# Kernel tuning notes

Hardware: AMD Instinct MI355X
Metric: run time of the kernel (lower is better)

The kernel has to match this reference:

```python
import jax, jax.numpy as jnp
import numpy as np

K = 1024
D = 64
BETA = 0.25


def setup_inputs() -> dict:
    key = jax.random.key(0)
    k1, k2 = jax.random.split(key)
    x = jax.random.normal(k1, (32, D, 64, 64), dtype=jnp.float32)
    # torch init: uniform(-1/K, 1/K)
    emb = jax.random.uniform(k2, (K, D), dtype=jnp.float32, minval=-1.0 / K, maxval=1.0 / K)
    return {"x": x, "emb": emb}


def reference(x, emb):
    B, C, H, W = x.shape
    z = jnp.transpose(x, (0, 2, 3, 1))          # [B,H,W,D]
    zf = z.reshape(-1, C)                        # [N,D]
    # squared euclidean distances ||z||^2 + ||e||^2 - 2 z.e
    dist = (jnp.sum(zf * zf, axis=1, keepdims=True)
            + jnp.sum(emb * emb, axis=1)
            - 2.0 * jnp.matmul(zf, emb.T))       # [N,K]
    min_idx = jnp.argmin(dist, axis=1)           # [N]
    # one-hot @ emb == gather
    z_q = emb[min_idx].reshape(z.shape)          # [B,H,W,D]
    sg = jax.lax.stop_gradient
    embedding_loss = (jnp.mean((sg(z_q) - z) ** 2)
                      + BETA * jnp.mean((z_q - sg(z)) ** 2))
    z_q_st = z + sg(z_q - z)                     # straight-through
    # code-usage perplexity
    n = zf.shape[0]
    e_mean = jnp.bincount(min_idx, length=K).astype(z.dtype) / n
    perplexity = jnp.exp(-jnp.sum(e_mean * jnp.log(e_mean + 1e-10)))
    z_q_out = jnp.transpose(z_q_st, (0, 3, 1, 2))  # [B,D,H,W]
    return embedding_loss, z_q_out, perplexity
```

## Files before the change

kernel.cpp:

```cpp
#include <hip/hip_runtime.h>
#include <math.h>

#define D_    64
#define K_    1024
#define N_    131072
#define HW_   4096
#define TAU   4e-5f

typedef unsigned long long ull;
typedef unsigned short ushort;
typedef short  bf16x8  __attribute__((ext_vector_type(8)));
typedef float  f32x4   __attribute__((ext_vector_type(4)));
typedef ushort ushort8 __attribute__((ext_vector_type(8)));

__device__ __forceinline__ ushort f2bf(float f) {
    unsigned u = __float_as_uint(f);
    return (ushort)((u + 0x7FFFu + ((u >> 16) & 1u)) >> 16);
}
__device__ __forceinline__ float b2f(ushort h) {
    return __uint_as_float((unsigned)h << 16);
}

__global__ __launch_bounds__(256)
void vq_prep(const float* __restrict__ emb, ushort* __restrict__ ehg,
             ushort* __restrict__ elg, float* __restrict__ e2g,
             float* __restrict__ embT, int* __restrict__ hist,
             int* __restrict__ cnt, double* __restrict__ ssqd) {
    const int n = blockIdx.x * 256 + threadIdx.x;
    if (n < K_) {
        const float* er = emb + (size_t)n * D_;
        float e2 = 0.0f;
        #pragma unroll
        for (int d8 = 0; d8 < 8; ++d8) {
            ushort8 hh, ll;
            #pragma unroll
            for (int j = 0; j < 8; ++j) {
                float e = er[d8 * 8 + j];
                e2 = fmaf(e, e, e2);
                ushort h = f2bf(e);
                hh[j] = h;
                ll[j] = f2bf(e - b2f(h));
                embT[(size_t)(d8 * 8 + j) * K_ + n] = e;
            }
            *(ushort8*)(ehg + (size_t)n * D_ + d8 * 8) = hh;
            *(ushort8*)(elg + (size_t)n * D_ + d8 * 8) = ll;
        }
        e2g[n] = e2;
        hist[n] = 0;
    }
    if (n == 0 && blockIdx.x == 0) { *cnt = 0; *ssqd = 0.0; }
}

#define LOADB(KT, BH0, BH1, BL0, BL1, E2)                                     \
    {                                                                         \
        int c_ = (kbase + (KT)) * 16 + c16;                                   \
        const ushort* eb_ = ehg + (size_t)c_ * D_ + g * 8;                    \
        BH0 = *(const bf16x8*)(eb_);                                          \
        BH1 = *(const bf16x8*)(eb_ + 32);                                     \
        const ushort* lb_ = elg + (size_t)c_ * D_ + g * 8;                    \
        BL0 = *(const bf16x8*)(lb_);                                          \
        BL1 = *(const bf16x8*)(lb_ + 32);                                     \
        E2 = e2g[c_];                                                         \
    }

#define COMPUTE(KT, BH0, BH1, BL0, BL1, E2)                                   \
    {                                                                         \
        const int c_ = (kbase + (KT)) * 16 + c16;                             \
        f32x4 ac[4];                                                          \
        _Pragma("unroll")                                                     \
        for (int t = 0; t < 4; ++t) {                                         \
            f32x4 a = {0.0f, 0.0f, 0.0f, 0.0f};                               \
            a = __builtin_amdgcn_mfma_f32_16x16x32_bf16(ah[t][0], BH0, a, 0, 0, 0); \
            a = __builtin_amdgcn_mfma_f32_16x16x32_bf16(al[t][0], BH0, a, 0, 0, 0); \
            a = __builtin_amdgcn_mfma_f32_16x16x32_bf16(ah[t][1], BH1, a, 0, 0, 0); \
            a = __builtin_amdgcn_mfma_f32_16x16x32_bf16(al[t][1], BH1, a, 0, 0, 0); \
            a = __builtin_amdgcn_mfma_f32_16x16x32_bf16(ah[t][0], BL0, a, 0, 0, 0); \
            a = __builtin_amdgcn_mfma_f32_16x16x32_bf16(ah[t][1], BL1, a, 0, 0, 0); \
            ac[t] = a;                                                        \
        }                                                                     \
        _Pragma("unroll")                                                     \
        for (int t = 0; t < 4; ++t) {                                         \
            _Pragma("unroll")                                                 \
            for (int q = 0; q < 4; ++q) {                                     \
                float dist = fmaf(-2.0f, ac[t][q], E2);                       \
                const int st = t * 4 + q;                                     \
                float vmax = fmaxf(dist, v1[st]);                             \
                bool lt = dist < v1[st];                                      \
                k1[st] = lt ? c_ : k1[st];                                    \
                v1[st] = fminf(dist, v1[st]);                                 \
                v2[st] = fminf(v2[st], vmax);                                 \
            }                                                                 \
        }                                                                     \
    }

__global__ __launch_bounds__(256)
void vq_mfma(const float* __restrict__ x, const float* __restrict__ emb,
             const ushort* __restrict__ ehg, const ushort* __restrict__ elg,
             const float* __restrict__ e2g, float* __restrict__ zq_out,
             int* __restrict__ list, int* __restrict__ cnt,
             int* __restrict__ hist, double* __restrict__ ssqd) {
    __shared__ float lv1[4][64], lv2[4][64];
    __shared__ int   lk1[4][64];
    __shared__ int   lkfin[128];

    const int tid = threadIdx.x;
    const int wv  = tid >> 6;
    const int rg  = wv >> 1;
    const int kh  = wv & 1;
    const int l   = tid & 63;
    const int g   = l >> 4;
    const int c16 = l & 15;
    const int n0b = blockIdx.x * 128;
    const int n0w = n0b + rg * 64;
    const int kbase = kh * 32;

    bf16x8 ah[4][2], al[4][2];
    #pragma unroll
    for (int t = 0; t < 4; ++t) {
        const int row = n0w + t * 16 + c16;
        const int b = row >> 12, hw = row & (HW_ - 1);
        const float* xr = x + (size_t)b * (D_ * HW_) + hw;
        #pragma unroll
        for (int s = 0; s < 2; ++s) {
            #pragma unroll
            for (int j = 0; j < 8; ++j) {
                float z = xr[(size_t)(g * 8 + s * 32 + j) * HW_];
                ushort h = f2bf(z);
                ah[t][s][j] = (short)h;
                al[t][s][j] = (short)f2bf(z - b2f(h));
            }
        }
    }

    float v1[16], v2[16]; int k1[16];
    #pragma unroll
    for (int st = 0; st < 16; ++st) { v1[st] = 3.4e38f; v2[st] = 3.4e38f; k1[st] = 0; }

    bf16x8 pbh0, pbh1, pbl0, pbl1; float pe2;
    LOADB(0, pbh0, pbh1, pbl0, pbl1, pe2)
    for (int kt = 0; kt < 32; kt += 2) {
        bf16x8 qbh0, qbh1, qbl0, qbl1; float qe2;
        LOADB(kt + 1, qbh0, qbh1, qbl0, qbl1, qe2)
        COMPUTE(kt, pbh0, pbh1, pbl0, pbl1, pe2)
        const int ktn = (kt + 2 < 32) ? kt + 2 : 31;
        LOADB(ktn, pbh0, pbh1, pbl0, pbl1, pe2)
        COMPUTE(kt + 1, qbh0, qbh1, qbl0, qbl1, qe2)
    }

    #pragma unroll
    for (int off = 1; off < 16; off <<= 1) {
        #pragma unroll
        for (int st = 0; st < 16; ++st) {
            float w1 = __shfl_xor(v1[st], off, 64);
            float w2 = __shfl_xor(v2[st], off, 64);
            int   wk = __shfl_xor(k1[st], off, 64);
            float lose = (w1 < v1[st]) ? v1[st] : w1;
            v2[st] = fminf(fminf(v2[st], w2), lose);
            if (w1 < v1[st]) { v1[st] = w1; k1[st] = wk; }
        }
    }

    if (c16 == 0) {
        #pragma unroll
        for (int t = 0; t < 4; ++t) {
            #pragma unroll
            for (int q = 0; q < 4; ++q) {
                const int st = t * 4 + q;
                const int rr = t * 16 + 4 * g + q;
                lv1[wv][rr] = v1[st];
                lv2[wv][rr] = v2[st];
                lk1[wv][rr] = k1[st];
            }
        }
    }
    __syncthreads();

    if (tid < 128) {
        const int rgm = tid >> 6, rr = tid & 63;
        const float a1 = lv1[rgm * 2 + 0][rr], b1 = lv1[rgm * 2 + 1][rr];
        const float a2 = lv2[rgm * 2 + 0][rr], b2 = lv2[rgm * 2 + 1][rr];
        float v1m; int k1m;
        if (b1 < a1) { v1m = b1; k1m = lk1[rgm * 2 + 1][rr]; }
        else         { v1m = a1; k1m = lk1[rgm * 2 + 0][rr]; }
        const float v2m = fminf(fmaxf(a1, b1), fminf(a2, b2));
        int kk;
        if (!(v2m - v1m > TAU)) {
            int i = atomicAdd(cnt, 1);
            list[i] = n0b + tid;
            kk = -1;
        } else {
            kk = k1m;
            atomicAdd(&hist[kk], 1);
        }
        lkfin[tid] = kk;
    }
    __syncthreads();

    const int lr = tid & 127;
    const int dh = tid >> 7;
    const int n  = n0b + lr;
    const int b2_ = n >> 12, hw2 = n & (HW_ - 1);
    const float* xr2  = x      + (size_t)b2_ * (D_ * HW_) + hw2;
    float*       outr = zq_out + (size_t)b2_ * (D_ * HW_) + hw2;
    const int kk = lkfin[lr];
    float ls = 0.0f;
    if (kk >= 0) {
        const float* er = emb + (size_t)kk * D_ + dh * 32;
        #pragma unroll
        for (int dd = 0; dd < 32; ++dd) {
            const int d = dh * 32 + dd;
            float zv = xr2[(size_t)d * HW_];
            float t  = er[dd] - zv;
            ls = fmaf(t, t, ls);
            outr[(size_t)d * HW_] = zv + t;
        }
    }
    #pragma unroll
    for (int o = 32; o > 0; o >>= 1) ls += __shfl_down(ls, o, 64);
    if (l == 0) atomicAdd(ssqd, (double)ls);
}

__global__ __launch_bounds__(256)
void vq_exact(const float* __restrict__ x, const float* __restrict__ emb,
              const float* __restrict__ embT, const float* __restrict__ e2g,
              const int* __restrict__ list, const int* __restrict__ cnt,
              float* __restrict__ zq_out, int* __restrict__ hist,
              double* __restrict__ ssqd) {
    const int l  = threadIdx.x & 63;
    const int gw = (blockIdx.x * 256 + threadIdx.x) >> 6;
    const int nw = (gridDim.x * 256) >> 6;
    const int C  = *cnt;
    for (int i = gw; i < C; i += nw) {
        const int n = list[i];
        const int b = n >> 12, hw = n & (HW_ - 1);
        const float* xr = x + (size_t)b * (D_ * HW_) + hw;
        const float zval = xr[(size_t)l * HW_];
        float r2 = 0.0f;
        float s[16];
        #pragma unroll
        for (int j = 0; j < 16; ++j) s[j] = 0.0f;
        for (int d = 0; d < D_; ++d) {
            const float zd = __shfl(zval, d, 64);
            r2 = fmaf(zd, zd, r2);
            const float* erow = embT + (size_t)d * K_ + l * 4;
            const float4 e0 = *(const float4*)(erow);
            const float4 e1 = *(const float4*)(erow + 256);
            const float4 e2 = *(const float4*)(erow + 512);
            const float4 e3 = *(const float4*)(erow + 768);
            s[0]  = fmaf(zd, e0.x, s[0]);  s[1]  = fmaf(zd, e0.y, s[1]);
            s[2]  = fmaf(zd, e0.z, s[2]);  s[3]  = fmaf(zd, e0.w, s[3]);
            s[4]  = fmaf(zd, e1.x, s[4]);  s[5]  = fmaf(zd, e1.y, s[5]);
            s[6]  = fmaf(zd, e1.z, s[6]);  s[7]  = fmaf(zd, e1.w, s[7]);
            s[8]  = fmaf(zd, e2.x, s[8]);  s[9]  = fmaf(zd, e2.y, s[9]);
            s[10] = fmaf(zd, e2.z, s[10]); s[11] = fmaf(zd, e2.w, s[11]);
            s[12] = fmaf(zd, e3.x, s[12]); s[13] = fmaf(zd, e3.y, s[13]);
            s[14] = fmaf(zd, e3.z, s[14]); s[15] = fmaf(zd, e3.w, s[15]);
        }
        ull best = ~0ull;
        #pragma unroll
        for (int j = 0; j < 16; ++j) {
            const int k = (j >> 2) * 256 + l * 4 + (j & 3);
            float dist = fmaf(-2.0f, s[j], r2 + e2g[k]);
            ull p = ((ull)__float_as_uint(dist) << 32) | (unsigned)k;
            if (p < best) best = p;
        }
        #pragma unroll
        for (int off = 1; off < 64; off <<= 1) {
            ull q = __shfl_xor(best, off, 64);
            if (q < best) best = q;
        }
        const int k = (int)(best & 0xffffffffull);
        const float e = emb[(size_t)k * D_ + l];
        const float t = e - zval;
        float ps = t * t;
        float* outr = zq_out + (size_t)b * (D_ * HW_) + hw;
        outr[(size_t)l * HW_] = zval + t;
        #pragma unroll
        for (int off = 32; off > 0; off >>= 1) ps += __shfl_down(ps, off, 64);
        if (l == 0) {
            atomicAdd(&hist[k], 1);
            atomicAdd(ssqd, (double)ps);
        }
    }
}

__global__ __launch_bounds__(1024)
void vq_final(const int* __restrict__ hist, const double* __restrict__ ssqd,
              float* __restrict__ out_loss, float* __restrict__ out_perp) {
    __shared__ float wred[16];
    int t = threadIdx.x;
    float cnt = (float)hist[t];
    float em  = cnt / (float)N_;
    float s   = em * logf(em + 1e-10f);
    #pragma unroll
    for (int o = 32; o > 0; o >>= 1) s += __shfl_down(s, o, 64);
    if ((t & 63) == 0) wred[t >> 6] = s;
    __syncthreads();
    if (t == 0) {
        float tot = 0.0f;
        for (int w = 0; w < 16; ++w) tot += wred[w];
        *out_perp = expf(-tot);
        float mse = (float)(*ssqd / (double)((size_t)N_ * D_));
        *out_loss = mse + 0.25f * mse;
    }
}

extern "C" void kernel_launch(void* const* d_in, const int* in_sizes, int n_in,
                              void* d_out, int out_size, void* d_ws, size_t ws_size,
                              hipStream_t stream) {
    const float* x   = (const float*)d_in[0];
    const float* emb = (const float*)d_in[1];
    float* out  = (float*)d_out;
    float* loss = out;
    float* zq   = out + 1;
    float* perp = out + 1 + (size_t)N_ * D_;

    char* w = (char*)d_ws;
    int*    list = (int*)w;     w += (size_t)N_ * 4;
    ushort* ehg  = (ushort*)w;  w += (size_t)K_ * D_ * 2;
    ushort* elg  = (ushort*)w;  w += (size_t)K_ * D_ * 2;
    float*  embT = (float*)w;   w += (size_t)K_ * D_ * 4;
    float*  e2g  = (float*)w;   w += (size_t)K_ * 4;
    int*    hist = (int*)w;     w += (size_t)K_ * 4;
    int*    cnt  = (int*)w;     w += 16;
    double* ssqd = (double*)w;

    vq_prep<<<dim3(4), dim3(256), 0, stream>>>(emb, ehg, elg, e2g, embT, hist, cnt, ssqd);
    vq_mfma<<<dim3(N_ / 128), dim3(256), 0, stream>>>(x, emb, ehg, elg, e2g, zq, list, cnt, hist, ssqd);
    vq_exact<<<dim3(2048), dim3(256), 0, stream>>>(x, emb, embT, e2g, list, cnt, zq, hist, ssqd);
    vq_final<<<dim3(1), dim3(1024), 0, stream>>>(hist, ssqd, loss, perp);
}
```

Before: 169.6 us.

## Stage codebook tiles in shared memory and give each wave all codes

```diff
diff --git a/kernel.cpp b/kernel.cpp
--- a/kernel.cpp
+++ b/kernel.cpp
@@ -6,6 +6,7 @@
 #define N_    131072
 #define HW_   4096
 #define TAU   4e-5f
+#define NKT   64
 
 typedef unsigned long long ull;
 typedef unsigned short ushort;
@@ -51,68 +52,28 @@
     if (n == 0 && blockIdx.x == 0) { *cnt = 0; *ssqd = 0.0; }
 }
 
-#define LOADB(KT, BH0, BH1, BL0, BL1, E2)                                     \
-    {                                                                         \
-        int c_ = (kbase + (KT)) * 16 + c16;                                   \
-        const ushort* eb_ = ehg + (size_t)c_ * D_ + g * 8;                    \
-        BH0 = *(const bf16x8*)(eb_);                                          \
-        BH1 = *(const bf16x8*)(eb_ + 32);                                     \
-        const ushort* lb_ = elg + (size_t)c_ * D_ + g * 8;                    \
-        BL0 = *(const bf16x8*)(lb_);                                          \
-        BL1 = *(const bf16x8*)(lb_ + 32);                                     \
-        E2 = e2g[c_];                                                         \
-    }
-
-#define COMPUTE(KT, BH0, BH1, BL0, BL1, E2)                                   \
-    {                                                                         \
-        const int c_ = (kbase + (KT)) * 16 + c16;                             \
-        f32x4 ac[4];                                                          \
-        _Pragma("unroll")                                                     \
-        for (int t = 0; t < 4; ++t) {                                         \
-            f32x4 a = {0.0f, 0.0f, 0.0f, 0.0f};                               \
-            a = __builtin_amdgcn_mfma_f32_16x16x32_bf16(ah[t][0], BH0, a, 0, 0, 0); \
-            a = __builtin_amdgcn_mfma_f32_16x16x32_bf16(al[t][0], BH0, a, 0, 0, 0); \
-            a = __builtin_amdgcn_mfma_f32_16x16x32_bf16(ah[t][1], BH1, a, 0, 0, 0); \
-            a = __builtin_amdgcn_mfma_f32_16x16x32_bf16(al[t][1], BH1, a, 0, 0, 0); \
-            a = __builtin_amdgcn_mfma_f32_16x16x32_bf16(ah[t][0], BL0, a, 0, 0, 0); \
-            a = __builtin_amdgcn_mfma_f32_16x16x32_bf16(ah[t][1], BL1, a, 0, 0, 0); \
-            ac[t] = a;                                                        \
-        }                                                                     \
-        _Pragma("unroll")                                                     \
-        for (int t = 0; t < 4; ++t) {                                         \
-            _Pragma("unroll")                                                 \
-            for (int q = 0; q < 4; ++q) {                                     \
-                float dist = fmaf(-2.0f, ac[t][q], E2);                       \
-                const int st = t * 4 + q;                                     \
-                float vmax = fmaxf(dist, v1[st]);                             \
-                bool lt = dist < v1[st];                                      \
-                k1[st] = lt ? c_ : k1[st];                                    \
-                v1[st] = fminf(dist, v1[st]);                                 \
-                v2[st] = fminf(v2[st], vmax);                                 \
-            }                                                                 \
-        }                                                                     \
-    }
-
-__global__ __launch_bounds__(256)
+__global__ __launch_bounds__(256, 2)
 void vq_mfma(const float* __restrict__ x, const float* __restrict__ emb,
              const ushort* __restrict__ ehg, const ushort* __restrict__ elg,
              const float* __restrict__ e2g, float* __restrict__ zq_out,
              int* __restrict__ list, int* __restrict__ cnt,
              int* __restrict__ hist, double* __restrict__ ssqd) {
-    __shared__ float lv1[4][64], lv2[4][64];
-    __shared__ int   lk1[4][64];
-    __shared__ int   lkfin[128];
+    __shared__ ushort bst[2][2][8][16][8];
+    __shared__ int lkfin[256];
 
     const int tid = threadIdx.x;
     const int wv  = tid >> 6;
-    const int rg  = wv >> 1;
-    const int kh  = wv & 1;
     const int l   = tid & 63;
     const int g   = l >> 4;
     const int c16 = l & 15;
-    const int n0b = blockIdx.x * 128;
-    const int n0w = n0b + rg * 64;
-    const int kbase = kh * 32;
+    const int n0b = blockIdx.x * 256;
+    const int n0w = n0b + wv * 64;
+
+    const int sHalf = tid >> 7;
+    const int sS    = tid & 127;
+    const int sCode = sS >> 3;
+    const int sSeg  = sS & 7;
+    const ushort* sBase = (sHalf ? elg : ehg) + (size_t)sCode * D_ + sSeg * 8;
 
     bf16x8 ah[4][2], al[4][2];
     #pragma unroll
@@ -136,15 +97,53 @@
     #pragma unroll
     for (int st = 0; st < 16; ++st) { v1[st] = 3.4e38f; v2[st] = 3.4e38f; k1[st] = 0; }
 
-    bf16x8 pbh0, pbh1, pbl0, pbl1; float pe2;
-    LOADB(0, pbh0, pbh1, pbl0, pbl1, pe2)
-    for (int kt = 0; kt < 32; kt += 2) {
-        bf16x8 qbh0, qbh1, qbl0, qbl1; float qe2;
-        LOADB(kt + 1, qbh0, qbh1, qbl0, qbl1, qe2)
-        COMPUTE(kt, pbh0, pbh1, pbl0, pbl1, pe2)
-        const int ktn = (kt + 2 < 32) ? kt + 2 : 31;
-        LOADB(ktn, pbh0, pbh1, pbl0, pbl1, pe2)
-        COMPUTE(kt + 1, qbh0, qbh1, qbl0, qbl1, qe2)
+    {
+        ushort8 pf = *(const ushort8*)(sBase);
+        *(ushort8*)(&bst[0][sHalf][sSeg][sCode][0]) = pf;
+    }
+    __syncthreads();
+
+    for (int kt = 0; kt < NKT; ++kt) {
+        const int cur = kt & 1;
+        const bool more = (kt + 1) < NKT;
+        ushort8 pf;
+        if (more) pf = *(const ushort8*)(sBase + (size_t)(kt + 1) * 16 * D_);
+
+        const bf16x8 bh0 = *(const bf16x8*)(&bst[cur][0][g    ][c16][0]);
+        const bf16x8 bh1 = *(const bf16x8*)(&bst[cur][0][g + 4][c16][0]);
+        const bf16x8 bl0 = *(const bf16x8*)(&bst[cur][1][g    ][c16][0]);
+        const bf16x8 bl1 = *(const bf16x8*)(&bst[cur][1][g + 4][c16][0]);
+        const int   c_  = kt * 16 + c16;
+        const float E2  = e2g[c_];
+
+        f32x4 ac[4];
+        #pragma unroll
+        for (int t = 0; t < 4; ++t) {
+            f32x4 a = {0.0f, 0.0f, 0.0f, 0.0f};
+            a = __builtin_amdgcn_mfma_f32_16x16x32_bf16(ah[t][0], bh0, a, 0, 0, 0);
+            a = __builtin_amdgcn_mfma_f32_16x16x32_bf16(al[t][0], bh0, a, 0, 0, 0);
+            a = __builtin_amdgcn_mfma_f32_16x16x32_bf16(ah[t][1], bh1, a, 0, 0, 0);
+            a = __builtin_amdgcn_mfma_f32_16x16x32_bf16(al[t][1], bh1, a, 0, 0, 0);
+            a = __builtin_amdgcn_mfma_f32_16x16x32_bf16(ah[t][0], bl0, a, 0, 0, 0);
+            a = __builtin_amdgcn_mfma_f32_16x16x32_bf16(ah[t][1], bl1, a, 0, 0, 0);
+            ac[t] = a;
+        }
+        #pragma unroll
+        for (int t = 0; t < 4; ++t) {
+            #pragma unroll
+            for (int q = 0; q < 4; ++q) {
+                float dist = fmaf(-2.0f, ac[t][q], E2);
+                const int st = t * 4 + q;
+                float vmax = fmaxf(dist, v1[st]);
+                bool lt = dist < v1[st];
+                k1[st] = lt ? c_ : k1[st];
+                v1[st] = fminf(dist, v1[st]);
+                v2[st] = fminf(v2[st], vmax);
+            }
+        }
+
+        if (more) *(ushort8*)(&bst[cur ^ 1][sHalf][sSeg][sCode][0]) = pf;
+        __syncthreads();
     }
 
     #pragma unroll
@@ -166,51 +165,34 @@
             #pragma unroll
             for (int q = 0; q < 4; ++q) {
                 const int st = t * 4 + q;
-                const int rr = t * 16 + 4 * g + q;
-                lv1[wv][rr] = v1[st];
-                lv2[wv][rr] = v2[st];
-                lk1[wv][rr] = k1[st];
+                const int rr = wv * 64 + t * 16 + 4 * g + q;
+                int kk;
+                if (!(v2[st] - v1[st] > TAU)) {
+                    int i = atomicAdd(cnt, 1);
+                    list[i] = n0b + rr;
+                    kk = -1;
+                } else {
+                    kk = k1[st];
+                    atomicAdd(&hist[kk], 1);
+                }
+                lkfin[rr] = kk;
             }
         }
     }
     __syncthreads();
 
-    if (tid < 128) {
-        const int rgm = tid >> 6, rr = tid & 63;
-        const float a1 = lv1[rgm * 2 + 0][rr], b1 = lv1[rgm * 2 + 1][rr];
-        const float a2 = lv2[rgm * 2 + 0][rr], b2 = lv2[rgm * 2 + 1][rr];
-        float v1m; int k1m;
-        if (b1 < a1) { v1m = b1; k1m = lk1[rgm * 2 + 1][rr]; }
-        else         { v1m = a1; k1m = lk1[rgm * 2 + 0][rr]; }
-        const float v2m = fminf(fmaxf(a1, b1), fminf(a2, b2));
-        int kk;
-        if (!(v2m - v1m > TAU)) {
-            int i = atomicAdd(cnt, 1);
-            list[i] = n0b + tid;
-            kk = -1;
-        } else {
-            kk = k1m;
-            atomicAdd(&hist[kk], 1);
-        }
-        lkfin[tid] = kk;
-    }
-    __syncthreads();
-
-    const int lr = tid & 127;
-    const int dh = tid >> 7;
-    const int n  = n0b + lr;
+    const int n  = n0b + tid;
     const int b2_ = n >> 12, hw2 = n & (HW_ - 1);
     const float* xr2  = x      + (size_t)b2_ * (D_ * HW_) + hw2;
     float*       outr = zq_out + (size_t)b2_ * (D_ * HW_) + hw2;
-    const int kk = lkfin[lr];
+    const int kk = lkfin[tid];
     float ls = 0.0f;
     if (kk >= 0) {
-        const float* er = emb + (size_t)kk * D_ + dh * 32;
-        #pragma unroll
-        for (int dd = 0; dd < 32; ++dd) {
-            const int d = dh * 32 + dd;
+        const float* er = emb + (size_t)kk * D_;
+        #pragma unroll
+        for (int d = 0; d < D_; ++d) {
             float zv = xr2[(size_t)d * HW_];
-            float t  = er[dd] - zv;
+            float t  = er[d] - zv;
             ls = fmaf(t, t, ls);
             outr[(size_t)d * HW_] = zv + t;
         }
@@ -326,7 +308,7 @@
     double* ssqd = (double*)w;
 
     vq_prep<<<dim3(4), dim3(256), 0, stream>>>(emb, ehg, elg, e2g, embT, hist, cnt, ssqd);
-    vq_mfma<<<dim3(N_ / 128), dim3(256), 0, stream>>>(x, emb, ehg, elg, e2g, zq, list, cnt, hist, ssqd);
+    vq_mfma<<<dim3(N_ / 256), dim3(256), 0, stream>>>(x, emb, ehg, elg, e2g, zq, list, cnt, hist, ssqd);
     vq_exact<<<dim3(2048), dim3(256), 0, stream>>>(x, emb, embT, e2g, list, cnt, zq, hist, ssqd);
     vq_final<<<dim3(1), dim3(1024), 0, stream>>>(hist, ssqd, loss, perp);
 }
```

New measurement: 158.3 us. 6.7% less time.

## Stage codebook tiles through double-buffered LDS with register prefetch

Applied to the files above, without the earlier changes.

```diff
diff --git a/kernel.cpp b/kernel.cpp
--- a/kernel.cpp
+++ b/kernel.cpp
@@ -6,6 +6,7 @@
 #define N_    131072
 #define HW_   4096
 #define TAU   4e-5f
+#define NST   32
 
 typedef unsigned long long ull;
 typedef unsigned short ushort;
@@ -19,6 +20,12 @@
 }
 __device__ __forceinline__ float b2f(ushort h) {
     return __uint_as_float((unsigned)h << 16);
+}
+#define SLOT(seg, code) ((seg) * 16 + ((code) ^ (seg)))
+
+__device__ __forceinline__ void block_sync_lds() {
+    asm volatile("s_waitcnt lgkmcnt(0)" ::: "memory");
+    __builtin_amdgcn_s_barrier();
 }
 
 __global__ __launch_bounds__(256)
@@ -51,33 +58,27 @@
     if (n == 0 && blockIdx.x == 0) { *cnt = 0; *ssqd = 0.0; }
 }
 
-#define LOADB(KT, BH0, BH1, BL0, BL1, E2)                                     \
+#define STEP(CUR, S, PFA, PFB)                                                \
     {                                                                         \
-        int c_ = (kbase + (KT)) * 16 + c16;                                   \
-        const ushort* eb_ = ehg + (size_t)c_ * D_ + g * 8;                    \
-        BH0 = *(const bf16x8*)(eb_);                                          \
-        BH1 = *(const bf16x8*)(eb_ + 32);                                     \
-        const ushort* lb_ = elg + (size_t)c_ * D_ + g * 8;                    \
-        BL0 = *(const bf16x8*)(lb_);                                          \
-        BL1 = *(const bf16x8*)(lb_ + 32);                                     \
-        E2 = e2g[c_];                                                         \
-    }
-
-#define COMPUTE(KT, BH0, BH1, BL0, BL1, E2)                                   \
-    {                                                                         \
-        const int c_ = (kbase + (KT)) * 16 + c16;                             \
+        const bf16x8 bh0 = *(const bf16x8*)(&bst[CUR][kh][0][SLOT(g,     c16)][0]); \
+        const bf16x8 bh1 = *(const bf16x8*)(&bst[CUR][kh][0][SLOT(g + 4, c16)][0]); \
+        const bf16x8 bl0 = *(const bf16x8*)(&bst[CUR][kh][1][SLOT(g,     c16)][0]); \
+        const bf16x8 bl1 = *(const bf16x8*)(&bst[CUR][kh][1][SLOT(g + 4, c16)][0]); \
+        const int   c_  = (kh * NST + (S)) * 16 + c16;                        \
+        const float E2  = e2g[c_];                                            \
         f32x4 ac[4];                                                          \
         _Pragma("unroll")                                                     \
         for (int t = 0; t < 4; ++t) {                                         \
             f32x4 a = {0.0f, 0.0f, 0.0f, 0.0f};                               \
-            a = __builtin_amdgcn_mfma_f32_16x16x32_bf16(ah[t][0], BH0, a, 0, 0, 0); \
-            a = __builtin_amdgcn_mfma_f32_16x16x32_bf16(al[t][0], BH0, a, 0, 0, 0); \
-            a = __builtin_amdgcn_mfma_f32_16x16x32_bf16(ah[t][1], BH1, a, 0, 0, 0); \
-            a = __builtin_amdgcn_mfma_f32_16x16x32_bf16(al[t][1], BH1, a, 0, 0, 0); \
-            a = __builtin_amdgcn_mfma_f32_16x16x32_bf16(ah[t][0], BL0, a, 0, 0, 0); \
-            a = __builtin_amdgcn_mfma_f32_16x16x32_bf16(ah[t][1], BL1, a, 0, 0, 0); \
+            a = __builtin_amdgcn_mfma_f32_16x16x32_bf16(ah[t][0], bh0, a, 0, 0, 0); \
+            a = __builtin_amdgcn_mfma_f32_16x16x32_bf16(al[t][0], bh0, a, 0, 0, 0); \
+            a = __builtin_amdgcn_mfma_f32_16x16x32_bf16(ah[t][1], bh1, a, 0, 0, 0); \
+            a = __builtin_amdgcn_mfma_f32_16x16x32_bf16(al[t][1], bh1, a, 0, 0, 0); \
+            a = __builtin_amdgcn_mfma_f32_16x16x32_bf16(ah[t][0], bl0, a, 0, 0, 0); \
+            a = __builtin_amdgcn_mfma_f32_16x16x32_bf16(ah[t][1], bl1, a, 0, 0, 0); \
             ac[t] = a;                                                        \
         }                                                                     \
+         \
         _Pragma("unroll")                                                     \
         for (int t = 0; t < 4; ++t) {                                         \
             _Pragma("unroll")                                                 \
@@ -91,14 +92,24 @@
                 v2[st] = fminf(v2[st], vmax);                                 \
             }                                                                 \
         }                                                                     \
-    }
-
-__global__ __launch_bounds__(256)
+        if ((S) + 1 < NST) {                                                  \
+            *(ushort8*)(&bst[(CUR) ^ 1][0][sHalf][s0Slot][0]) = PFA;          \
+            *(ushort8*)(&bst[(CUR) ^ 1][1][sHalf][s1Slot][0]) = PFB;          \
+        }                                                                     \
+        if ((S) + 3 < NST) {                                                  \
+            PFA = *(const ushort8*)(s0Base + (size_t)((S) + 3) * 16 * D_);    \
+            PFB = *(const ushort8*)(s1Base + (size_t)((S) + 3) * 16 * D_);    \
+        }                                                                     \
+        block_sync_lds();                                                     \
+    }
+
+__global__ __launch_bounds__(256, 2)
 void vq_mfma(const float* __restrict__ x, const float* __restrict__ emb,
              const ushort* __restrict__ ehg, const ushort* __restrict__ elg,
              const float* __restrict__ e2g, float* __restrict__ zq_out,
              int* __restrict__ list, int* __restrict__ cnt,
              int* __restrict__ hist, double* __restrict__ ssqd) {
+    __shared__ ushort bst[2][2][2][128][8];
     __shared__ float lv1[4][64], lv2[4][64];
     __shared__ int   lk1[4][64];
     __shared__ int   lkfin[128];
@@ -112,7 +123,15 @@
     const int c16 = l & 15;
     const int n0b = blockIdx.x * 128;
     const int n0w = n0b + rg * 64;
-    const int kbase = kh * 32;
+
+    const int sHalf = tid >> 7;
+    const int sS    = tid & 127;
+    const int sCode = sS >> 3;
+    const int sSeg  = sS & 7;
+    const int s0Slot = SLOT(sSeg, sCode);
+    const int s1Slot = s0Slot;
+    const ushort* s0Base = (sHalf ? elg : ehg) + (size_t)sCode * D_ + sSeg * 8;
+    const ushort* s1Base = s0Base + (size_t)NST * 16 * D_;
 
     bf16x8 ah[4][2], al[4][2];
     #pragma unroll
@@ -136,15 +155,18 @@
     #pragma unroll
     for (int st = 0; st < 16; ++st) { v1[st] = 3.4e38f; v2[st] = 3.4e38f; k1[st] = 0; }
 
-    bf16x8 pbh0, pbh1, pbl0, pbl1; float pe2;
-    LOADB(0, pbh0, pbh1, pbl0, pbl1, pe2)
-    for (int kt = 0; kt < 32; kt += 2) {
-        bf16x8 qbh0, qbh1, qbl0, qbl1; float qe2;
-        LOADB(kt + 1, qbh0, qbh1, qbl0, qbl1, qe2)
-        COMPUTE(kt, pbh0, pbh1, pbl0, pbl1, pe2)
-        const int ktn = (kt + 2 < 32) ? kt + 2 : 31;
-        LOADB(ktn, pbh0, pbh1, pbl0, pbl1, pe2)
-        COMPUTE(kt + 1, qbh0, qbh1, qbl0, qbl1, qe2)
+    *(ushort8*)(&bst[0][0][sHalf][s0Slot][0]) = *(const ushort8*)(s0Base);
+    *(ushort8*)(&bst[0][1][sHalf][s1Slot][0]) = *(const ushort8*)(s1Base);
+    ushort8 pf0a = *(const ushort8*)(s0Base + (size_t)1 * 16 * D_);
+    ushort8 pf0b = *(const ushort8*)(s1Base + (size_t)1 * 16 * D_);
+    ushort8 pf1a = *(const ushort8*)(s0Base + (size_t)2 * 16 * D_);
+    ushort8 pf1b = *(const ushort8*)(s1Base + (size_t)2 * 16 * D_);
+    block_sync_lds();
+
+    #pragma unroll 1
+    for (int s = 0; s < NST; s += 2) {
+        STEP(0, s,     pf0a, pf0b)
+        STEP(1, s + 1, pf1a, pf1b)
     }
 
     #pragma unroll
```

After: 154.9 us. 1.1x faster.
